# Performance work log

Hardware: AMD Instinct MI355X
Metric: run time of the kernel (lower is better)

Reference implementation:

```python
import math
import jax, jax.numpy as jnp
import numpy as np

N, E, D, B, S, H = 16384, 196608, 256, 256, 64, 8
DH = D // H
BN_INV = 1.0 / math.sqrt(1.0 + 1e-5)  # eval-mode BN: mean=0, var=1, eps=1e-5
LOG2 = math.log(2.0)


def _mlp(x, w1, b1, w2, b2):
    # Linear -> SiLU -> Linear
    return jax.nn.silu(x @ w1 + b1) @ w2 + b2


def _bn(x, g, b):
    # BatchNorm1d in eval mode with running_mean=0, running_var=1
    return x * (BN_INV * g) + b


def _graph_ln(x, g, b):
    # pyg LayerNorm(mode='graph') called with batch=None: normalize over all nodes+features
    mu = jnp.mean(x)
    xc = x - mu
    var = jnp.mean(xc * xc)
    return xc * jax.lax.rsqrt(var + 1e-5) * g + b


def _forward(x, edge_index, edge_attr,
             node_w1, node_b1, node_w2, node_b2,
             c_w1, c_b1, c_w2, c_b2,
             bn_e_g, bn_e_b, bn_h_g, bn_h_b,
             n1l_g, n1l_b, n1a_g, n1a_b, n2_g, n2_b,
             wq, bq, wk, bk, wv, bv, wo, bo,
             aff_w1, aff_b1, aff_w2, aff_b2,
             fn_g, fn_b, fc_w1, fc_b1, fc_w2, fc_b2):
    row, col = edge_index[0], edge_index[1]

    # ---- PotNetConvGate local branch ----
    # A, B, V, U MLPs (all take node features) computed with stacked weights [4,D,D]
    hid = jax.nn.silu(jnp.einsum('nd,kdf->knf', x, node_w1) + node_b1[:, None, :])
    node_out = jnp.einsum('knf,kfg->kng', hid, node_w2) + node_b2[:, None, :]
    h_A, h_B, h_V, h_U = node_out[0], node_out[1], node_out[2], node_out[3]
    e_C = _mlp(edge_attr, c_w1, c_b1, c_w2, c_b2)  # [E,D]

    score = jax.nn.relu(_bn(h_A[row] + h_B[col] + e_C, bn_e_g, bn_e_b))  # [E,D]
    e_new = edge_attr + score

    # pyg softmax over edges grouped by destination node (col), per channel
    m = jax.ops.segment_max(e_new, col, num_segments=N)        # [N,D]
    ex = jnp.exp(e_new - m[col])
    s = jax.ops.segment_sum(ex, col, num_segments=N)           # [N,D]
    gated = ex / (s[col] + 1e-16)

    msg = gated * (h_V[col] + e_new)
    aggr = jax.ops.segment_sum(msg, col, num_segments=N)       # [N,D]
    h_local = jax.nn.silu(x + _bn(h_U + aggr, bn_h_g, bn_h_b))
    # e_out = silu(e_new + edge_attr)  # edge output, not used downstream for node output
    h_local = _bn(h_local, n1l_g, n1l_b)  # norm1_local

    # ---- global Transformer branch (equal-size graphs -> dense reshape, full mask) ----
    hd = x.reshape(B, S, D)
    q = (hd @ wq + bq).reshape(B, S, H, DH).transpose(0, 2, 1, 3)
    k = (hd @ wk + bk).reshape(B, S, H, DH).transpose(0, 2, 1, 3)
    v = (hd @ wv + bv).reshape(B, S, H, DH).transpose(0, 2, 1, 3)
    att = jax.nn.softmax(jnp.einsum('bhqd,bhkd->bhqk', q, k) / math.sqrt(DH), axis=-1)
    o = jnp.einsum('bhqk,bhkd->bhqd', att, v).transpose(0, 2, 1, 3).reshape(B, S, D)
    h_attn = (o @ wo + bo).reshape(N, D)

    h_attn = _bn(h_attn + x, n1a_g, n1a_b)  # norm1_attn
    t = jax.nn.gelu(h_attn @ aff_w1 + aff_b1, approximate=False) @ aff_w2 + aff_b2
    h_attn = _graph_ln(t + x, fn_g, fn_b)   # feed_norm

    # ---- fuse branches (mean over stacked outputs) ----
    h_new = (h_local + h_attn) * 0.5

    # ---- _ff_block: fc = Linear -> ShiftedSoftplus -> Linear ----
    ssp = jax.nn.softplus(h_new @ fc_w1 + fc_b1) - LOG2
    out = ssp @ fc_w2 + fc_b2
    return _bn(out + h_new, n2_g, n2_b)  # norm2


def setup_inputs():
    key = jax.random.key(0)
    ks = iter(jax.random.split(key, 64))
    sc = 1.0 / math.sqrt(D)
    def w(shape):
        return jax.random.normal(next(ks), shape, jnp.float32) * sc
    z = lambda *s: jnp.zeros(s, jnp.float32)
    o = lambda *s: jnp.ones(s, jnp.float32)
    return {
        'x': jax.random.normal(next(ks), (N, D), jnp.float32),
        'edge_index': jax.random.randint(next(ks), (2, E), 0, N, jnp.int32),
        'edge_attr': jax.random.normal(next(ks), (E, D), jnp.float32),
        'node_w1': w((4, D, D)), 'node_b1': z(4, D),
        'node_w2': w((4, D, D)), 'node_b2': z(4, D),
        'c_w1': w((D, D)), 'c_b1': z(D), 'c_w2': w((D, D)), 'c_b2': z(D),
        'bn_e_g': o(D), 'bn_e_b': z(D), 'bn_h_g': o(D), 'bn_h_b': z(D),
        'n1l_g': o(D), 'n1l_b': z(D), 'n1a_g': o(D), 'n1a_b': z(D),
        'n2_g': o(D), 'n2_b': z(D),
        'wq': w((D, D)), 'bq': z(D), 'wk': w((D, D)), 'bk': z(D),
        'wv': w((D, D)), 'bv': z(D), 'wo': w((D, D)), 'bo': z(D),
        'aff_w1': w((D, 2 * D)), 'aff_b1': z(2 * D),
        'aff_w2': w((2 * D, D)), 'aff_b2': z(D),
        'fn_g': o(D), 'fn_b': z(D),
        'fc_w1': w((D, 2 * D)), 'fc_b1': z(2 * D),
        'fc_w2': w((2 * D, D)), 'fc_b2': z(D),
    }


def reference(x, edge_index, edge_attr,
              node_w1, node_b1, node_w2, node_b2,
              c_w1, c_b1, c_w2, c_b2,
              bn_e_g, bn_e_b, bn_h_g, bn_h_b,
              n1l_g, n1l_b, n1a_g, n1a_b, n2_g, n2_b,
              wq, bq, wk, bk, wv, bv, wo, bo,
              aff_w1, aff_b1, aff_w2, aff_b2,
              fn_g, fn_b, fc_w1, fc_b1, fc_w2, fc_b2):
    return _forward(x, edge_index, edge_attr,
                    node_w1, node_b1, node_w2, node_b2,
                    c_w1, c_b1, c_w2, c_b2,
                    bn_e_g, bn_e_b, bn_h_g, bn_h_b,
                    n1l_g, n1l_b, n1a_g, n1a_b, n2_g, n2_b,
                    wq, bq, wk, bk, wv, bv, wo, bo,
                    aff_w1, aff_b1, aff_w2, aff_b2,
                    fn_g, fn_b, fc_w1, fc_b1, fc_w2, fc_b2)
```

## Files before the change

### kernel.cpp

```cpp
#include <hip/hip_runtime.h>
#include <hip/hip_bf16.h>
#include <stdint.h>

#define NN 16384
#define NE 196608
#define DD 256
#define ND 4194304
#define BNINV 0.9999950000374997f
#define LOG2F_ 0.6931471805599453f

typedef __attribute__((ext_vector_type(8))) short short8v;
typedef __attribute__((ext_vector_type(4))) float float4v;

__device__ __forceinline__ float b2f(__hip_bfloat16 v) { return __bfloat162float(v); }
__device__ __forceinline__ __hip_bfloat16 f2b(float v) { return __float2bfloat16(v); }

__device__ __forceinline__ void gl_lds16(const __hip_bfloat16* g, __hip_bfloat16* l) {
  __builtin_amdgcn_global_load_lds((const __attribute__((address_space(1))) void*)g,
                                   (__attribute__((address_space(3))) void*)l, 16, 0, 0);
}

__device__ __forceinline__ float rdf(const void* p, size_t i, int fl) {
  return fl ? b2f(((const __hip_bfloat16*)p)[i]) : ((const float*)p)[i];
}

#define OFF_WT    0ul
#define OFF_PB    2883584ul
#define OFF_XB    2899968ul
#define OFF_HN    11288576ul
#define OFF_HL    44843008ul
#define OFF_EN    162283520ul
#define OFF_QKV   262946816ul
#define OFF_O     313278464ul
#define OFF_HATTN 321667072ul
#define OFF_HIDN  330055680ul
#define OFF_U     346832896ul
#define OFF_HNEW  363610112ul
#define OFF_HNEWB 380387328ul
#define OFF_TAIL  388775936ul

#define PB_NB1   0
#define PB_NB2   1024
#define PB_CB1   2048
#define PB_CB2   2304
#define PB_QKVB  2560
#define PB_BO    3328
#define PB_AB1   3584
#define PB_AB2   4096
#define PB_FB1   4352
#define PB_FB2   4864
#define PB_BNEG  5120
#define PB_BNEB  5376
#define PB_BNHG  5632
#define PB_BNHB  5888
#define PB_N1LG  6144
#define PB_N1LB  6400
#define PB_N1AG  6656
#define PB_N1AB  6912
#define PB_N2G   7168
#define PB_N2B   7424
#define PB_FNG   7680
#define PB_FNB   7936

__global__ void probe_kernel(const uint32_t* bneg_raw, int* flag) {
  if (threadIdx.x == 0 && blockIdx.x == 0)
    *flag = (bneg_raw[0] == 0x3F803F80u) ? 1 : 0;
}

struct PJobs {
  const void* src[24];
  int off[24];
  int len[24];
};

__global__ void canon_params(PJobs jb, __hip_bfloat16* PB, const int* flagp) {
  const int fl = *flagp;
  const int j = blockIdx.x;
  const void* src = jb.src[j];
  const int off = jb.off[j], len = jb.len[j];
  for (int i = threadIdx.x; i < len; i += 256) PB[off + i] = f2b(rdf(src, i, fl));
}

__global__ void canon_x(const void* x, __hip_bfloat16* XB, const int* flagp) {
  const int fl = *flagp;
  const size_t i = (size_t)blockIdx.x * 256 + threadIdx.x;
  XB[i] = f2b(rdf(x, i, fl));
}

struct TJobsF {
  const void* src[18];
  __hip_bfloat16* dst[18];
  int R[18];
  int C[18];
  int RB[18];
};

__global__ void transpose_rb(TJobsF jb, const int* flagp) {
  __shared__ __hip_bfloat16 tile[32][33];
  const int fl = *flagp;
  const int j = blockIdx.z;
  const int R = jb.R[j], C = jb.C[j], RB = jb.RB[j];
  const int c0 = blockIdx.x * 32, r0 = blockIdx.y * 32;
  if (c0 >= C || r0 >= R) return;
  const void* src = jb.src[j];
  __hip_bfloat16* dst = jb.dst[j];
  const int tx = threadIdx.x, ty = threadIdx.y;
#pragma unroll
  for (int i = 0; i < 4; ++i)
    tile[ty + i * 8][tx] = f2b(rdf(src, (size_t)(RB + r0 + ty + i * 8) * C + c0 + tx, fl));
  __syncthreads();
#pragma unroll
  for (int i = 0; i < 4; ++i)
    dst[(long)(c0 + ty + i * 8) * R + r0 + tx] = tile[tx][ty + i * 8];
}

__global__ void prep_kernel(int* counts, double* stats) {
  const int i = blockIdx.x * blockDim.x + threadIdx.x;
  if (i < NN) counts[i] = 0;
  if (i == 0) counts[NN] = 0;
  if (i < 2) stats[i] = 0.0;
}

template <int ACT, int RES, int BNM, int OUTBF, int DUALOUT>
__global__ __launch_bounds__(256) void gemm_bt(
    const void* __restrict__ Avp, const __hip_bfloat16* __restrict__ Wt,
    const __hip_bfloat16* __restrict__ bias, const void* __restrict__ Res,
    const __hip_bfloat16* __restrict__ bng, const __hip_bfloat16* __restrict__ bnb,
    void* __restrict__ Cout, const int* __restrict__ flagp,
    int M, int N, int K, long boff, long az, long wz, long bz, long cz) {
  __shared__ __align__(16) __hip_bfloat16 sA[128 * 32];
  __shared__ __align__(16) __hip_bfloat16 sB[128 * 32];
  const int fl = DUALOUT ? *flagp : 1;
  const int z = blockIdx.z;
  const long aoff = boff + (long)z * az;
  const __hip_bfloat16* Ab = (const __hip_bfloat16*)Avp + aoff;
  Wt += (long)z * wz;
  bias += (long)z * bz;
  const long coff = (long)z * cz;
  const int tid = threadIdx.x;
  const int lane = tid & 63;
  const int wid = tid >> 6;
  const int wm = wid >> 1, wn = wid & 1;
  const int l16 = lane & 15, lq = lane >> 4;
  const long am0 = (long)blockIdx.y * 128;
  const long bn0 = (long)blockIdx.x * 128;

  float4v acc[4][4] = {};

  const int nK = K >> 5;
  for (int kb = 0; kb < nK; ++kb) {
#pragma unroll
    for (int r = 0; r < 2; ++r) {
      const int c = tid + r * 256;
      gl_lds16(Ab + (am0 + (c >> 2)) * K + kb * 32 + (c & 3) * 8, sA + c * 8);
      gl_lds16(Wt + (bn0 + (c >> 2)) * K + kb * 32 + (c & 3) * 8, sB + c * 8);
    }
    __syncthreads();
    const short* pA = (const short*)sA;
    const short* pB = (const short*)sB;
    short8v af[4], bv_[4];
#pragma unroll
    for (int mi = 0; mi < 4; ++mi)
      af[mi] = *(const short8v*)(pA + (wm * 64 + mi * 16 + l16) * 32 + lq * 8);
#pragma unroll
    for (int ni = 0; ni < 4; ++ni)
      bv_[ni] = *(const short8v*)(pB + (wn * 64 + ni * 16 + l16) * 32 + lq * 8);
#pragma unroll
    for (int mi = 0; mi < 4; ++mi)
#pragma unroll
      for (int ni = 0; ni < 4; ++ni)
        acc[mi][ni] =
            __builtin_amdgcn_mfma_f32_16x16x32_bf16(af[mi], bv_[ni], acc[mi][ni], 0, 0, 0);
    __syncthreads();
  }

  const __hip_bfloat16* Rb = (const __hip_bfloat16*)Res;
  const float* Rf = (const float*)Res;
#pragma unroll
  for (int mi = 0; mi < 4; ++mi) {
#pragma unroll
    for (int ni = 0; ni < 4; ++ni) {
#pragma unroll
      for (int r = 0; r < 4; ++r) {
        const long row = am0 + wm * 64 + mi * 16 + lq * 4 + r;
        const long col = bn0 + wn * 64 + ni * 16 + l16;
        float v = acc[mi][ni][r] + b2f(bias[col]);
        if (ACT == 1) v = v / (1.f + __expf(-v));
        else if (ACT == 2) v = 0.5f * v * (1.f + erff(v * 0.7071067811865476f));
        else if (ACT == 3) v = (v > 15.f ? v : log1pf(__expf(v))) - LOG2F_;
        if (RES == 1) v += b2f(Rb[row * N + col]);
        else if (RES == 2) v += Rf[row * N + col];
        if (BNM) v = v * (BNINV * b2f(bng[col])) + b2f(bnb[col]);
        if (DUALOUT) {
          if (fl) ((__hip_bfloat16*)Cout)[coff + row * N + col] = f2b(v);
          else ((float*)Cout)[coff + row * N + col] = v;
        } else if (OUTBF) {
          ((__hip_bfloat16*)Cout)[coff + row * N + col] = f2b(v);
        } else {
          ((float*)Cout)[coff + row * N + col] = v;
        }
      }
    }
  }
}

template <int EPI, int ASRC>
__global__ __launch_bounds__(256) void mlp_fused(
    const void* __restrict__ Avp, const __hip_bfloat16* __restrict__ W1t,
    const __hip_bfloat16* __restrict__ b1, const __hip_bfloat16* __restrict__ W2t,
    const __hip_bfloat16* __restrict__ b2, __hip_bfloat16* __restrict__ Out,
    const int* __restrict__ ei, const void* __restrict__ eattr,
    const __hip_bfloat16* __restrict__ HA, __hip_bfloat16* __restrict__ EN,
    const __hip_bfloat16* __restrict__ PB, const int* __restrict__ perm,
    const int* __restrict__ flagp, long wz, long cz) {
  __shared__ __align__(16) __hip_bfloat16 sW[256 * 32];
  __shared__ __align__(16) __hip_bfloat16 sH[64 * 264];
  const int fl = (ASRC == 1) ? *flagp : 1;
  const int z = blockIdx.z;
  W1t += (long)z * wz;
  W2t += (long)z * wz;
  b1 += z * 256;
  b2 += z * 256;
  const int tid = threadIdx.x;
  const int lane = tid & 63;
  const int wn = tid >> 6;
  const int l16 = lane & 15, lq = lane >> 4;
  const long m0 = (long)blockIdx.y * 64;
  const __hip_bfloat16* Ab = (const __hip_bfloat16*)Avp;
  const float* Af = (const float*)Avp;

  float4v acc[4][4] = {};

  for (int kb = 0; kb < 8; ++kb) {
    if (ASRC == 1 && fl == 0) {
      const int arow = tid >> 2, ko = (tid & 3) * 8;
      const float* ap = Af + (m0 + arow) * 256 + kb * 32 + ko;
      const float4v f0 = *(const float4v*)ap;
      const float4v f1 = *(const float4v*)(ap + 4);
      short8v s;
#pragma unroll
      for (int i = 0; i < 4; ++i) {
        __hip_bfloat16 h0 = f2b(f0[i]), h1 = f2b(f1[i]);
        s[i] = *(short*)&h0;
        s[4 + i] = *(short*)&h1;
      }
      ((short8v*)sH)[tid] = s;
    } else {
      gl_lds16(Ab + (m0 + (tid >> 2)) * 256 + kb * 32 + (tid & 3) * 8, sH + tid * 8);
    }
#pragma unroll
    for (int r = 0; r < 4; ++r) {
      const int c2 = r * 256 + tid;
      gl_lds16(W1t + (c2 >> 2) * 256 + kb * 32 + (c2 & 3) * 8, sW + c2 * 8);
    }
    __syncthreads();
    short8v af[4], bf_[4];
#pragma unroll
    for (int mi = 0; mi < 4; ++mi)
      af[mi] = *(const short8v*)((const short*)sH + (mi * 16 + l16) * 32 + lq * 8);
#pragma unroll
    for (int ni = 0; ni < 4; ++ni)
      bf_[ni] = *(const short8v*)((const short*)sW + (wn * 64 + ni * 16 + l16) * 32 + lq * 8);
#pragma unroll
    for (int mi = 0; mi < 4; ++mi)
#pragma unroll
      for (int ni = 0; ni < 4; ++ni)
        acc[mi][ni] =
            __builtin_amdgcn_mfma_f32_16x16x32_bf16(af[mi], bf_[ni], acc[mi][ni], 0, 0, 0);
    __syncthreads();
  }

  {
    short* hp = (short*)sH;
#pragma unroll
    for (int mi = 0; mi < 4; ++mi)
#pragma unroll
      for (int ni = 0; ni < 4; ++ni)
#pragma unroll
        for (int r = 0; r < 4; ++r) {
          const int row = mi * 16 + lq * 4 + r;
          const int col = wn * 64 + ni * 16 + l16;
          float v = acc[mi][ni][r] + b2f(b1[col]);
          v = v / (1.f + __expf(-v));
          __hip_bfloat16 hb = f2b(v);
          hp[row * 264 + col] = *(short*)&hb;
          acc[mi][ni][r] = 0.f;
        }
  }
  __syncthreads();

  for (int kb = 0; kb < 8; ++kb) {
#pragma unroll
    for (int r = 0; r < 4; ++r) {
      const int c2 = r * 256 + tid;
      gl_lds16(W2t + (c2 >> 2) * 256 + kb * 32 + (c2 & 3) * 8, sW + c2 * 8);
    }
    __syncthreads();
    short8v af[4], bf_[4];
#pragma unroll
    for (int mi = 0; mi < 4; ++mi)
      af[mi] = *(const short8v*)((const short*)sH + (mi * 16 + l16) * 264 + kb * 32 + lq * 8);
#pragma unroll
    for (int ni = 0; ni < 4; ++ni)
      bf_[ni] = *(const short8v*)((const short*)sW + (wn * 64 + ni * 16 + l16) * 32 + lq * 8);
#pragma unroll
    for (int mi = 0; mi < 4; ++mi)
#pragma unroll
      for (int ni = 0; ni < 4; ++ni)
        acc[mi][ni] =
            __builtin_amdgcn_mfma_f32_16x16x32_bf16(af[mi], bf_[ni], acc[mi][ni], 0, 0, 0);
    __syncthreads();
  }

  if (EPI == 0) {
#pragma unroll
    for (int mi = 0; mi < 4; ++mi)
#pragma unroll
      for (int ni = 0; ni < 4; ++ni)
#pragma unroll
        for (int r = 0; r < 4; ++r) {
          const long row = m0 + mi * 16 + lq * 4 + r;
          const int col = wn * 64 + ni * 16 + l16;
          Out[(long)z * cz + row * 256 + col] = f2b(acc[mi][ni][r] + b2f(b2[col]));
        }
  } else {
    const __hip_bfloat16* HB = HA + (size_t)ND;
#pragma unroll
    for (int mi = 0; mi < 4; ++mi)
#pragma unroll
      for (int r = 0; r < 4; ++r) {
        const long ge = m0 + mi * 16 + lq * 4 + r;
        const int rr = ei[ge];
        const int cc = ei[NE + ge];
        const long pe = perm[ge];
#pragma unroll
        for (int ni = 0; ni < 4; ++ni) {
          const int col = wn * 64 + ni * 16 + l16;
          float v = acc[mi][ni][r] + b2f(b2[col]);
          v += b2f(HA[(size_t)rr * DD + col]) + b2f(HB[(size_t)cc * DD + col]);
          v = v * (BNINV * b2f(PB[PB_BNEG + col])) + b2f(PB[PB_BNEB + col]);
          v = fmaxf(v, 0.f);
          v += rdf(eattr, (size_t)ge * DD + col, fl);
          EN[(size_t)pe * DD + col] = f2b(v);
        }
      }
  }
}

__global__ void count_kernel(const int* __restrict__ ei, int* __restrict__ counts) {
  const int e = blockIdx.x * 256 + threadIdx.x;
  if (e < NE) atomicAdd(&counts[ei[NE + e]], 1);
}

__global__ __launch_bounds__(1024) void scan_kernel(int* __restrict__ counts,
                                                    int* __restrict__ cursor) {
  __shared__ int part[1024];
  const int t = threadIdx.x;
  const int base = t * 16;
  int ss = 0;
#pragma unroll
  for (int i = 0; i < 16; ++i) ss += counts[base + i];
  part[t] = ss;
  __syncthreads();
  for (int off = 1; off < 1024; off <<= 1) {
    int v = (t >= off) ? part[t - off] : 0;
    __syncthreads();
    part[t] += v;
    __syncthreads();
  }
  int run = part[t] - ss;
  for (int i = 0; i < 16; ++i) {
    const int cv = counts[base + i];
    counts[base + i] = run;
    cursor[base + i] = run;
    run += cv;
  }
  if (t == 1023) counts[NN] = run;
}

__global__ void scatter_kernel(const int* __restrict__ ei, int* __restrict__ cursor,
                               int* __restrict__ perm) {
  const int e = blockIdx.x * 256 + threadIdx.x;
  if (e < NE) {
    const int p = atomicAdd(&cursor[ei[NE + e]], 1);
    perm[e] = p;
  }
}

__global__ __launch_bounds__(256) void segment_kernel(
    const int* __restrict__ offs, const __hip_bfloat16* __restrict__ EN,
    const __hip_bfloat16* __restrict__ hV, const __hip_bfloat16* __restrict__ hU,
    const __hip_bfloat16* __restrict__ XB, const __hip_bfloat16* __restrict__ PB,
    float* __restrict__ hlocal) {
  const int n = blockIdx.x;
  const int d = threadIdx.x;
  const int beg = offs[n], end = offs[n + 1];
  float sa = 0.f, sb = 0.f;
  int p = beg;
  for (; p + 4 <= end; p += 4) {
    const float v0 = b2f(EN[(size_t)(p + 0) * DD + d]);
    const float v1 = b2f(EN[(size_t)(p + 1) * DD + d]);
    const float v2 = b2f(EN[(size_t)(p + 2) * DD + d]);
    const float v3 = b2f(EN[(size_t)(p + 3) * DD + d]);
    const float e0 = __expf(v0), e1 = __expf(v1), e2 = __expf(v2), e3 = __expf(v3);
    sa += (e0 + e1) + (e2 + e3);
    sb += (e0 * v0 + e1 * v1) + (e2 * v2 + e3 * v3);
  }
  for (; p < end; ++p) {
    const float v = b2f(EN[(size_t)p * DD + d]);
    const float e = __expf(v);
    sa += e;
    sb += e * v;
  }
  const float hv = b2f(hV[(size_t)n * DD + d]);
  const float ag = (hv * sa + sb) / (sa + 1e-16f);
  const float t1 =
      (b2f(hU[(size_t)n * DD + d]) + ag) * (BNINV * b2f(PB[PB_BNHG + d])) + b2f(PB[PB_BNHB + d]);
  float s1 = b2f(XB[(size_t)n * DD + d]) + t1;
  s1 = s1 / (1.f + __expf(-s1));
  s1 = s1 * (BNINV * b2f(PB[PB_N1LG + d])) + b2f(PB[PB_N1LB + d]);
  hlocal[(size_t)n * DD + d] = s1;
}

__global__ __launch_bounds__(256) void attn_kernel(const float* __restrict__ QKV,
                                                   __hip_bfloat16* __restrict__ O) {
  __shared__ float sq[64][33], sk[64][33], sv[64][33];
  __shared__ float sp[64][65];
  const int bh = blockIdx.x;
  const int b = bh >> 3, h = bh & 7;
  const int tid = threadIdx.x;
  const float* Q = QKV;
  const float* Kp = QKV + (size_t)ND;
  const float* Vp = QKV + 2 * (size_t)ND;
#pragma unroll
  for (int j = 0; j < 8; ++j) {
    const int idx = j * 256 + tid;
    const int s = idx >> 5, dh = idx & 31;
    const size_t ga = ((size_t)(b * 64 + s)) * DD + h * 32 + dh;
    sq[s][dh] = Q[ga];
    sk[s][dh] = Kp[ga];
    sv[s][dh] = Vp[ga];
  }
  __syncthreads();
  const int row = tid >> 2, l4 = tid & 3;
  float qr[32];
#pragma unroll
  for (int d = 0; d < 32; ++d) qr[d] = sq[row][d];
  float sc[16];
  float mx = -1e30f;
#pragma unroll
  for (int jj = 0; jj < 16; ++jj) {
    const int j = l4 * 16 + jj;
    float dot = 0.f;
#pragma unroll
    for (int d = 0; d < 32; ++d) dot += qr[d] * sk[j][d];
    dot *= 0.17677669529663687f;
    sc[jj] = dot;
    mx = fmaxf(mx, dot);
  }
  mx = fmaxf(mx, __shfl_xor(mx, 1));
  mx = fmaxf(mx, __shfl_xor(mx, 2));
  float se = 0.f;
#pragma unroll
  for (int jj = 0; jj < 16; ++jj) {
    sc[jj] = __expf(sc[jj] - mx);
    se += sc[jj];
  }
  se += __shfl_xor(se, 1);
  se += __shfl_xor(se, 2);
  const float inv = 1.f / se;
#pragma unroll
  for (int jj = 0; jj < 16; ++jj) sp[row][l4 * 16 + jj] = sc[jj] * inv;
  __syncthreads();
#pragma unroll
  for (int k8 = 0; k8 < 8; ++k8) {
    const int dh = l4 * 8 + k8;
    float acc = 0.f;
#pragma unroll
    for (int j = 0; j < 64; ++j) acc += sp[row][j] * sv[j][dh];
    O[((size_t)(b * 64 + row)) * DD + h * 32 + dh] = f2b(acc);
  }
}

__global__ __launch_bounds__(256) void stats_kernel(const float* __restrict__ U,
                                                    double* __restrict__ st) {
  double s = 0.0, s2 = 0.0;
  for (size_t i = (size_t)blockIdx.x * 256 + threadIdx.x; i < (size_t)ND;
       i += (size_t)gridDim.x * 256) {
    const double v = (double)U[i];
    s += v;
    s2 += v * v;
  }
  for (int o = 32; o > 0; o >>= 1) {
    s += __shfl_down(s, o);
    s2 += __shfl_down(s2, o);
  }
  __shared__ double wred[4][2];
  const int lane = threadIdx.x & 63, w = threadIdx.x >> 6;
  if (lane == 0) {
    wred[w][0] = s;
    wred[w][1] = s2;
  }
  __syncthreads();
  if (threadIdx.x == 0) {
    double a = 0, bb = 0;
    for (int i = 0; i < 4; ++i) {
      a += wred[i][0];
      bb += wred[i][1];
    }
    atomicAdd(&st[0], a);
    atomicAdd(&st[1], bb);
  }
}

__global__ void finalize_stats(double* st) {
  if (threadIdx.x == 0 && blockIdx.x == 0) {
    const double mu = st[0] / (double)ND;
    const double var = st[1] / (double)ND - mu * mu;
    float* f = (float*)(st + 2);
    f[0] = (float)mu;
    f[1] = (float)(1.0 / sqrt(var + 1e-5));
  }
}

__global__ void hnew_kernel(const float* __restrict__ U, const float* __restrict__ hlocal,
                            const double* __restrict__ st, const __hip_bfloat16* __restrict__ PB,
                            float* __restrict__ HNEW, __hip_bfloat16* __restrict__ HNEWB) {
  const size_t i = (size_t)blockIdx.x * 256 + threadIdx.x;
  const float* f = (const float*)(st + 2);
  const float mu = f[0], rs = f[1];
  const int d = (int)(i & 255);
  const float ha = (U[i] - mu) * rs * b2f(PB[PB_FNG + d]) + b2f(PB[PB_FNB + d]);
  const float hn = 0.5f * (hlocal[i] + ha);
  HNEW[i] = hn;
  HNEWB[i] = f2b(hn);
}

extern "C" void kernel_launch(void* const* d_in, const int* in_sizes, int n_in, void* d_out,
                              int out_size, void* d_ws, size_t ws_size, hipStream_t stream) {
  (void)in_sizes; (void)n_in; (void)out_size; (void)ws_size;
  const void* x = d_in[0];
  const int* ei = (const int*)d_in[1];
  const void* eattr = d_in[2];

  uint8_t* ws = (uint8_t*)d_ws;
  __hip_bfloat16* WT = (__hip_bfloat16*)(ws + OFF_WT);
  __hip_bfloat16* PB = (__hip_bfloat16*)(ws + OFF_PB);
  __hip_bfloat16* XB = (__hip_bfloat16*)(ws + OFF_XB);
  __hip_bfloat16* HN = (__hip_bfloat16*)(ws + OFF_HN);
  float* HL = (float*)(ws + OFF_HL);
  __hip_bfloat16* EN = (__hip_bfloat16*)(ws + OFF_EN);
  float* QKV = (float*)(ws + OFF_QKV);
  __hip_bfloat16* O = (__hip_bfloat16*)(ws + OFF_O);
  __hip_bfloat16* HATTN = (__hip_bfloat16*)(ws + OFF_HATTN);
  __hip_bfloat16* HIDN = (__hip_bfloat16*)(ws + OFF_HIDN);
  float* U = (float*)(ws + OFF_U);
  float* HNEW = (float*)(ws + OFF_HNEW);
  __hip_bfloat16* HNEWB = (__hip_bfloat16*)(ws + OFF_HNEWB);
  uint8_t* tail = ws + OFF_TAIL;
  int* counts = (int*)tail;
  int* cursor = (int*)(tail + 66048ul);
  int* perm = (int*)(tail + 132096ul);
  double* stats = (double*)(tail + 918528ul);
  int* flag = (int*)(tail + 918592ul);

  probe_kernel<<<1, 64, 0, stream>>>((const uint32_t*)d_in[11], flag);

  PJobs pj;
  {
    const int srcidx[24] = {4, 6, 8, 10, 22, 24, 26, 28, 30, 32, 36, 38,
                            11, 12, 13, 14, 15, 16, 17, 18, 19, 20, 33, 34};
    const int dstoff[24] = {PB_NB1, PB_NB2, PB_CB1, PB_CB2, PB_QKVB, PB_QKVB + 256,
                            PB_QKVB + 512, PB_BO, PB_AB1, PB_AB2, PB_FB1, PB_FB2,
                            PB_BNEG, PB_BNEB, PB_BNHG, PB_BNHB, PB_N1LG, PB_N1LB,
                            PB_N1AG, PB_N1AB, PB_N2G, PB_N2B, PB_FNG, PB_FNB};
    const int lens[24] = {1024, 1024, 256, 256, 256, 256, 256, 256, 512, 256, 512, 256,
                          256, 256, 256, 256, 256, 256, 256, 256, 256, 256, 256, 256};
    for (int i = 0; i < 24; ++i) {
      pj.src[i] = d_in[srcidx[i]];
      pj.off[i] = dstoff[i];
      pj.len[i] = lens[i];
    }
  }
  canon_params<<<24, 256, 0, stream>>>(pj, PB, flag);
  canon_x<<<NN, 256, 0, stream>>>(x, XB, flag);

  TJobsF jf;
  for (int j = 0; j < 4; ++j) {
    jf.src[j] = d_in[3]; jf.dst[j] = WT + j * 65536;
    jf.R[j] = 256; jf.C[j] = 256; jf.RB[j] = j * 256;
    jf.src[4 + j] = d_in[5]; jf.dst[4 + j] = WT + 262144 + j * 65536;
    jf.R[4 + j] = 256; jf.C[4 + j] = 256; jf.RB[4 + j] = j * 256;
  }
  {
    const int widx[10] = {7, 9, 21, 23, 25, 27, 29, 31, 35, 37};
    const long wdst[10] = {524288, 589824, 655360, 720896, 786432, 851968,
                           917504, 1048576, 1179648, 1310720};
    const int wR[10] = {256, 256, 256, 256, 256, 256, 256, 512, 256, 512};
    const int wC[10] = {256, 256, 256, 256, 256, 256, 512, 256, 512, 256};
    for (int j = 0; j < 10; ++j) {
      jf.src[8 + j] = d_in[widx[j]]; jf.dst[8 + j] = WT + wdst[j];
      jf.R[8 + j] = wR[j]; jf.C[8 + j] = wC[j]; jf.RB[8 + j] = 0;
    }
  }
  transpose_rb<<<dim3(16, 16, 18), dim3(32, 8), 0, stream>>>(jf, flag);

  prep_kernel<<<64, 256, 0, stream>>>(counts, stats);

  count_kernel<<<768, 256, 0, stream>>>(ei, counts);
  scan_kernel<<<1, 1024, 0, stream>>>(counts, cursor);
  scatter_kernel<<<768, 256, 0, stream>>>(ei, cursor, perm);

  mlp_fused<0, 0><<<dim3(1, 256, 4), 256, 0, stream>>>(
      XB, WT, PB + PB_NB1, WT + 262144, PB + PB_NB2, HN,
      nullptr, nullptr, nullptr, nullptr, nullptr, nullptr, flag, 65536, ND);

  mlp_fused<1, 1><<<dim3(1, 3072, 1), 256, 0, stream>>>(
      eattr, WT + 524288, PB + PB_CB1, WT + 589824, PB + PB_CB2, nullptr,
      ei, eattr, HN, EN, PB, perm, flag, 0, 0);

  segment_kernel<<<NN, 256, 0, stream>>>(counts, EN, HN + 2 * (size_t)ND,
                                         HN + 3 * (size_t)ND, XB, PB, HL);

  gemm_bt<0, 0, 0, 0, 0><<<dim3(2, 128, 3), 256, 0, stream>>>(
      XB, WT + 655360, PB + PB_QKVB, nullptr, nullptr, nullptr, QKV, flag,
      NN, DD, DD, 0, 0, 65536, 256, ND);
  attn_kernel<<<2048, 256, 0, stream>>>(QKV, O);
  gemm_bt<0, 1, 1, 1, 0><<<dim3(2, 128, 1), 256, 0, stream>>>(
      O, WT + 851968, PB + PB_BO, XB, PB + PB_N1AG, PB + PB_N1AB, HATTN, flag,
      NN, DD, DD, 0, 0, 0, 0, 0);

  gemm_bt<2, 0, 0, 1, 0><<<dim3(4, 128, 1), 256, 0, stream>>>(
      HATTN, WT + 917504, PB + PB_AB1, nullptr, nullptr, nullptr, HIDN, flag,
      NN, 512, DD, 0, 0, 0, 0, 0);
  gemm_bt<0, 1, 0, 0, 0><<<dim3(2, 128, 1), 256, 0, stream>>>(
      HIDN, WT + 1048576, PB + PB_AB2, XB, nullptr, nullptr, U, flag,
      NN, DD, 512, 0, 0, 0, 0, 0);

  stats_kernel<<<1024, 256, 0, stream>>>(U, stats);
  finalize_stats<<<1, 64, 0, stream>>>(stats);
  hnew_kernel<<<NN, 256, 0, stream>>>(U, HL, stats, PB, HNEW, HNEWB);

  gemm_bt<3, 0, 0, 1, 0><<<dim3(4, 128, 1), 256, 0, stream>>>(
      HNEWB, WT + 1179648, PB + PB_FB1, nullptr, nullptr, nullptr, HIDN, flag,
      NN, 512, DD, 0, 0, 0, 0, 0);
  gemm_bt<0, 2, 1, 1, 1><<<dim3(2, 128, 1), 256, 0, stream>>>(
      HIDN, WT + 1310720, PB + PB_FB2, HNEW, PB + PB_N2G, PB + PB_N2B, d_out, flag,
      NN, DD, 512, 0, 0, 0, 0, 0);
}
```

Baseline: 899.2 us.

## Load MFMA fragments directly from global memory instead of staging through LDS

Both the generic GEMM and the fused MLP kernel stop copying A and weight tiles into shared memory with global_load_lds. Each wave now reads its MFMA operand fragments straight from global memory into registers, which removes the per-K-step barriers and LDS traffic, and the loops are unrolled by two. In exchange, operand tiles shared across waves are fetched redundantly through the caches, and the strided 16-byte row reads may coalesce less well.

```diff
diff --git a/kernel.cpp b/kernel.cpp
--- a/kernel.cpp
+++ b/kernel.cpp
@@ -14,11 +14,6 @@
 
 __device__ __forceinline__ float b2f(__hip_bfloat16 v) { return __bfloat162float(v); }
 __device__ __forceinline__ __hip_bfloat16 f2b(float v) { return __float2bfloat16(v); }
-
-__device__ __forceinline__ void gl_lds16(const __hip_bfloat16* g, __hip_bfloat16* l) {
-  __builtin_amdgcn_global_load_lds((const __attribute__((address_space(1))) void*)g,
-                                   (__attribute__((address_space(3))) void*)l, 16, 0, 0);
-}
 
 __device__ __forceinline__ float rdf(const void* p, size_t i, int fl) {
   return fl ? b2f(((const __hip_bfloat16*)p)[i]) : ((const float*)p)[i];
@@ -128,8 +123,6 @@
     const __hip_bfloat16* __restrict__ bng, const __hip_bfloat16* __restrict__ bnb,
     void* __restrict__ Cout, const int* __restrict__ flagp,
     int M, int N, int K, long boff, long az, long wz, long bz, long cz) {
-  __shared__ __align__(16) __hip_bfloat16 sA[128 * 32];
-  __shared__ __align__(16) __hip_bfloat16 sB[128 * 32];
   const int fl = DUALOUT ? *flagp : 1;
   const int z = blockIdx.z;
   const long aoff = boff + (long)z * az;
@@ -148,30 +141,21 @@
   float4v acc[4][4] = {};
 
   const int nK = K >> 5;
+#pragma unroll 2
   for (int kb = 0; kb < nK; ++kb) {
-#pragma unroll
-    for (int r = 0; r < 2; ++r) {
-      const int c = tid + r * 256;
-      gl_lds16(Ab + (am0 + (c >> 2)) * K + kb * 32 + (c & 3) * 8, sA + c * 8);
-      gl_lds16(Wt + (bn0 + (c >> 2)) * K + kb * 32 + (c & 3) * 8, sB + c * 8);
-    }
-    __syncthreads();
-    const short* pA = (const short*)sA;
-    const short* pB = (const short*)sB;
     short8v af[4], bv_[4];
 #pragma unroll
     for (int mi = 0; mi < 4; ++mi)
-      af[mi] = *(const short8v*)(pA + (wm * 64 + mi * 16 + l16) * 32 + lq * 8);
+      af[mi] = *(const short8v*)(Ab + (am0 + wm * 64 + mi * 16 + l16) * K + kb * 32 + lq * 8);
 #pragma unroll
     for (int ni = 0; ni < 4; ++ni)
-      bv_[ni] = *(const short8v*)(pB + (wn * 64 + ni * 16 + l16) * 32 + lq * 8);
+      bv_[ni] = *(const short8v*)(Wt + (bn0 + wn * 64 + ni * 16 + l16) * K + kb * 32 + lq * 8);
 #pragma unroll
     for (int mi = 0; mi < 4; ++mi)
 #pragma unroll
       for (int ni = 0; ni < 4; ++ni)
         acc[mi][ni] =
             __builtin_amdgcn_mfma_f32_16x16x32_bf16(af[mi], bv_[ni], acc[mi][ni], 0, 0, 0);
-    __syncthreads();
   }
 
   const __hip_bfloat16* Rb = (const __hip_bfloat16*)Res;
@@ -213,7 +197,6 @@
     const __hip_bfloat16* __restrict__ HA, __hip_bfloat16* __restrict__ EN,
     const __hip_bfloat16* __restrict__ PB, const int* __restrict__ perm,
     const int* __restrict__ flagp, long wz, long cz) {
-  __shared__ __align__(16) __hip_bfloat16 sW[256 * 32];
   __shared__ __align__(16) __hip_bfloat16 sH[64 * 264];
   const int fl = (ASRC == 1) ? *flagp : 1;
   const int z = blockIdx.z;
@@ -231,43 +214,38 @@
 
   float4v acc[4][4] = {};
 
+#pragma unroll 2
   for (int kb = 0; kb < 8; ++kb) {
+    short8v af[4], bf_[4];
     if (ASRC == 1 && fl == 0) {
-      const int arow = tid >> 2, ko = (tid & 3) * 8;
-      const float* ap = Af + (m0 + arow) * 256 + kb * 32 + ko;
-      const float4v f0 = *(const float4v*)ap;
-      const float4v f1 = *(const float4v*)(ap + 4);
-      short8v s;
-#pragma unroll
-      for (int i = 0; i < 4; ++i) {
-        __hip_bfloat16 h0 = f2b(f0[i]), h1 = f2b(f1[i]);
-        s[i] = *(short*)&h0;
-        s[4 + i] = *(short*)&h1;
+#pragma unroll
+      for (int mi = 0; mi < 4; ++mi) {
+        const float* ap = Af + (m0 + mi * 16 + l16) * 256 + kb * 32 + lq * 8;
+        const float4v f0 = *(const float4v*)ap;
+        const float4v f1 = *(const float4v*)(ap + 4);
+        short8v s;
+#pragma unroll
+        for (int i = 0; i < 4; ++i) {
+          __hip_bfloat16 h0 = f2b(f0[i]), h1 = f2b(f1[i]);
+          s[i] = *(short*)&h0;
+          s[4 + i] = *(short*)&h1;
+        }
+        af[mi] = s;
       }
-      ((short8v*)sH)[tid] = s;
     } else {
-      gl_lds16(Ab + (m0 + (tid >> 2)) * 256 + kb * 32 + (tid & 3) * 8, sH + tid * 8);
+#pragma unroll
+      for (int mi = 0; mi < 4; ++mi)
+        af[mi] = *(const short8v*)(Ab + (m0 + mi * 16 + l16) * 256 + kb * 32 + lq * 8);
     }
 #pragma unroll
-    for (int r = 0; r < 4; ++r) {
-      const int c2 = r * 256 + tid;
-      gl_lds16(W1t + (c2 >> 2) * 256 + kb * 32 + (c2 & 3) * 8, sW + c2 * 8);
-    }
-    __syncthreads();
-    short8v af[4], bf_[4];
-#pragma unroll
-    for (int mi = 0; mi < 4; ++mi)
-      af[mi] = *(const short8v*)((const short*)sH + (mi * 16 + l16) * 32 + lq * 8);
-#pragma unroll
     for (int ni = 0; ni < 4; ++ni)
-      bf_[ni] = *(const short8v*)((const short*)sW + (wn * 64 + ni * 16 + l16) * 32 + lq * 8);
+      bf_[ni] = *(const short8v*)(W1t + (wn * 64 + ni * 16 + l16) * 256 + kb * 32 + lq * 8);
 #pragma unroll
     for (int mi = 0; mi < 4; ++mi)
 #pragma unroll
       for (int ni = 0; ni < 4; ++ni)
         acc[mi][ni] =
             __builtin_amdgcn_mfma_f32_16x16x32_bf16(af[mi], bf_[ni], acc[mi][ni], 0, 0, 0);
-    __syncthreads();
   }
 
   {
@@ -289,27 +267,21 @@
   }
   __syncthreads();
 
+#pragma unroll 2
   for (int kb = 0; kb < 8; ++kb) {
-#pragma unroll
-    for (int r = 0; r < 4; ++r) {
-      const int c2 = r * 256 + tid;
-      gl_lds16(W2t + (c2 >> 2) * 256 + kb * 32 + (c2 & 3) * 8, sW + c2 * 8);
-    }
-    __syncthreads();
     short8v af[4], bf_[4];
 #pragma unroll
     for (int mi = 0; mi < 4; ++mi)
       af[mi] = *(const short8v*)((const short*)sH + (mi * 16 + l16) * 264 + kb * 32 + lq * 8);
 #pragma unroll
     for (int ni = 0; ni < 4; ++ni)
-      bf_[ni] = *(const short8v*)((const short*)sW + (wn * 64 + ni * 16 + l16) * 32 + lq * 8);
+      bf_[ni] = *(const short8v*)(W2t + (wn * 64 + ni * 16 + l16) * 256 + kb * 32 + lq * 8);
 #pragma unroll
     for (int mi = 0; mi < 4; ++mi)
 #pragma unroll
       for (int ni = 0; ni < 4; ++ni)
         acc[mi][ni] =
             __builtin_amdgcn_mfma_f32_16x16x32_bf16(af[mi], bf_[ni], acc[mi][ni], 0, 0, 0);
-    __syncthreads();
   }
 
   if (EPI == 0) {
```

Result: slower. 1.322 ms (+47.1%).

## Double-buffer LDS tiles in gemm and fused MLP kernels to overlap loads

Applied to the files above, without the earlier changes.

Adds two-stage LDS buffering to the generic GEMM and the fused two-layer MLP kernel. The next K-slice of A and weights is issued into the alternate buffer before the MFMAs on the current slice, and one barrier per iteration replaces two. This is meant to hide global-to-LDS latency behind compute. The trade-off is doubled LDS use for the weight and tile buffers, which may lower occupancy. The fp32 input path is now prefetched into registers and converted after compute.

```diff
diff --git a/kernel.cpp b/kernel.cpp
--- a/kernel.cpp
+++ b/kernel.cpp
@@ -22,6 +22,26 @@
 
 __device__ __forceinline__ float rdf(const void* p, size_t i, int fl) {
   return fl ? b2f(((const __hip_bfloat16*)p)[i]) : ((const float*)p)[i];
+}
+
+__device__ __forceinline__ short8v cvt8(float4v f0, float4v f1) {
+  short8v s;
+#pragma unroll
+  for (int i = 0; i < 4; ++i) {
+    __hip_bfloat16 h0 = f2b(f0[i]), h1 = f2b(f1[i]);
+    s[i] = *(short*)&h0;
+    s[4 + i] = *(short*)&h1;
+  }
+  return s;
+}
+
+__device__ __forceinline__ void stage_w(const __hip_bfloat16* W, __hip_bfloat16* buf,
+                                        int kb, int tid) {
+#pragma unroll
+  for (int r = 0; r < 4; ++r) {
+    const int c2 = r * 256 + tid;
+    gl_lds16(W + (c2 >> 2) * 256 + kb * 32 + (c2 & 3) * 8, buf + c2 * 8);
+  }
 }
 
 #define OFF_WT    0ul
@@ -128,8 +148,8 @@
     const __hip_bfloat16* __restrict__ bng, const __hip_bfloat16* __restrict__ bnb,
     void* __restrict__ Cout, const int* __restrict__ flagp,
     int M, int N, int K, long boff, long az, long wz, long bz, long cz) {
-  __shared__ __align__(16) __hip_bfloat16 sA[128 * 32];
-  __shared__ __align__(16) __hip_bfloat16 sB[128 * 32];
+  __shared__ __align__(16) __hip_bfloat16 sA[2][128 * 32];
+  __shared__ __align__(16) __hip_bfloat16 sB[2][128 * 32];
   const int fl = DUALOUT ? *flagp : 1;
   const int z = blockIdx.z;
   const long aoff = boff + (long)z * az;
@@ -148,16 +168,27 @@
   float4v acc[4][4] = {};
 
   const int nK = K >> 5;
+#pragma unroll
+  for (int r = 0; r < 2; ++r) {
+    const int c = tid + r * 256;
+    gl_lds16(Ab + (am0 + (c >> 2)) * K + (c & 3) * 8, sA[0] + c * 8);
+    gl_lds16(Wt + (bn0 + (c >> 2)) * K + (c & 3) * 8, sB[0] + c * 8);
+  }
+  __syncthreads();
+
   for (int kb = 0; kb < nK; ++kb) {
-#pragma unroll
-    for (int r = 0; r < 2; ++r) {
-      const int c = tid + r * 256;
-      gl_lds16(Ab + (am0 + (c >> 2)) * K + kb * 32 + (c & 3) * 8, sA + c * 8);
-      gl_lds16(Wt + (bn0 + (c >> 2)) * K + kb * 32 + (c & 3) * 8, sB + c * 8);
+    const int cur = kb & 1;
+    if (kb + 1 < nK) {
+      const int nx = cur ^ 1;
+#pragma unroll
+      for (int r = 0; r < 2; ++r) {
+        const int c = tid + r * 256;
+        gl_lds16(Ab + (am0 + (c >> 2)) * K + (kb + 1) * 32 + (c & 3) * 8, sA[nx] + c * 8);
+        gl_lds16(Wt + (bn0 + (c >> 2)) * K + (kb + 1) * 32 + (c & 3) * 8, sB[nx] + c * 8);
+      }
     }
-    __syncthreads();
-    const short* pA = (const short*)sA;
-    const short* pB = (const short*)sB;
+    const short* pA = (const short*)sA[cur];
+    const short* pB = (const short*)sB[cur];
     short8v af[4], bv_[4];
 #pragma unroll
     for (int mi = 0; mi < 4; ++mi)
@@ -171,7 +202,7 @@
       for (int ni = 0; ni < 4; ++ni)
         acc[mi][ni] =
             __builtin_amdgcn_mfma_f32_16x16x32_bf16(af[mi], bv_[ni], acc[mi][ni], 0, 0, 0);
-    __syncthreads();
+    if (kb + 1 < nK) __syncthreads();
   }
 
   const __hip_bfloat16* Rb = (const __hip_bfloat16*)Res;
@@ -213,7 +244,7 @@
     const __hip_bfloat16* __restrict__ HA, __hip_bfloat16* __restrict__ EN,
     const __hip_bfloat16* __restrict__ PB, const int* __restrict__ perm,
     const int* __restrict__ flagp, long wz, long cz) {
-  __shared__ __align__(16) __hip_bfloat16 sW[256 * 32];
+  __shared__ __align__(16) __hip_bfloat16 sW[2][256 * 32];
   __shared__ __align__(16) __hip_bfloat16 sH[64 * 264];
   const int fl = (ASRC == 1) ? *flagp : 1;
   const int z = blockIdx.z;
@@ -228,45 +259,51 @@
   const long m0 = (long)blockIdx.y * 64;
   const __hip_bfloat16* Ab = (const __hip_bfloat16*)Avp;
   const float* Af = (const float*)Avp;
+  const int arow = tid >> 2, ako = (tid & 3) * 8;
 
   float4v acc[4][4] = {};
 
+  if (ASRC == 1 && fl == 0) {
+    const float* ap = Af + (m0 + arow) * 256 + ako;
+    ((short8v*)sH)[tid] = cvt8(*(const float4v*)ap, *(const float4v*)(ap + 4));
+  } else {
+    gl_lds16(Ab + (m0 + arow) * 256 + ako, sH + tid * 8);
+  }
+  stage_w(W1t, sW[0], 0, tid);
+  __syncthreads();
+
   for (int kb = 0; kb < 8; ++kb) {
-    if (ASRC == 1 && fl == 0) {
-      const int arow = tid >> 2, ko = (tid & 3) * 8;
-      const float* ap = Af + (m0 + arow) * 256 + kb * 32 + ko;
-      const float4v f0 = *(const float4v*)ap;
-      const float4v f1 = *(const float4v*)(ap + 4);
-      short8v s;
-#pragma unroll
-      for (int i = 0; i < 4; ++i) {
-        __hip_bfloat16 h0 = f2b(f0[i]), h1 = f2b(f1[i]);
-        s[i] = *(short*)&h0;
-        s[4 + i] = *(short*)&h1;
+    const int cur = kb & 1;
+    float4v pf0, pf1;
+    int pend = 0;
+    if (kb < 7) {
+      if (ASRC == 1 && fl == 0) {
+        const float* ap = Af + (m0 + arow) * 256 + (kb + 1) * 32 + ako;
+        pf0 = *(const float4v*)ap;
+        pf1 = *(const float4v*)(ap + 4);
+        pend = 1;
+      } else {
+        gl_lds16(Ab + (m0 + arow) * 256 + (kb + 1) * 32 + ako,
+                 sH + (cur ^ 1) * 2048 + tid * 8);
       }
-      ((short8v*)sH)[tid] = s;
-    } else {
-      gl_lds16(Ab + (m0 + (tid >> 2)) * 256 + kb * 32 + (tid & 3) * 8, sH + tid * 8);
+      stage_w(W1t, sW[cur ^ 1], kb + 1, tid);
     }
-#pragma unroll
-    for (int r = 0; r < 4; ++r) {
-      const int c2 = r * 256 + tid;
-      gl_lds16(W1t + (c2 >> 2) * 256 + kb * 32 + (c2 & 3) * 8, sW + c2 * 8);
-    }
-    __syncthreads();
+    const short* pA = (const short*)(sH + cur * 2048);
+    const short* pW = (const short*)sW[cur];
     short8v af[4], bf_[4];
 #pragma unroll
     for (int mi = 0; mi < 4; ++mi)
-      af[mi] = *(const short8v*)((const short*)sH + (mi * 16 + l16) * 32 + lq * 8);
+      af[mi] = *(const short8v*)(pA + (mi * 16 + l16) * 32 + lq * 8);
 #pragma unroll
     for (int ni = 0; ni < 4; ++ni)
-      bf_[ni] = *(const short8v*)((const short*)sW + (wn * 64 + ni * 16 + l16) * 32 + lq * 8);
+      bf_[ni] = *(const short8v*)(pW + (wn * 64 + ni * 16 + l16) * 32 + lq * 8);
 #pragma unroll
     for (int mi = 0; mi < 4; ++mi)
 #pragma unroll
       for (int ni = 0; ni < 4; ++ni)
         acc[mi][ni] =
             __builtin_amdgcn_mfma_f32_16x16x32_bf16(af[mi], bf_[ni], acc[mi][ni], 0, 0, 0);
+    if (pend) ((short8v*)(sH + (cur ^ 1) * 2048))[tid] = cvt8(pf0, pf1);
     __syncthreads();
   }
 
@@ -287,29 +324,27 @@
           acc[mi][ni][r] = 0.f;
         }
   }
+  stage_w(W2t, sW[0], 0, tid);
   __syncthreads();
 
   for (int kb = 0; kb < 8; ++kb) {
-#pragma unroll
-    for (int r = 0; r < 4; ++r) {
-      const int c2 = r * 256 + tid;
-      gl_lds16(W2t + (c2 >> 2) * 256 + kb * 32 + (c2 & 3) * 8, sW + c2 * 8);
-    }
-    __syncthreads();
+    const int cur = kb & 1;
+    if (kb < 7) stage_w(W2t, sW[cur ^ 1], kb + 1, tid);
+    const short* pW = (const short*)sW[cur];
     short8v af[4], bf_[4];
 #pragma unroll
     for (int mi = 0; mi < 4; ++mi)
       af[mi] = *(const short8v*)((const short*)sH + (mi * 16 + l16) * 264 + kb * 32 + lq * 8);
 #pragma unroll
     for (int ni = 0; ni < 4; ++ni)
-      bf_[ni] = *(const short8v*)((const short*)sW + (wn * 64 + ni * 16 + l16) * 32 + lq * 8);
+      bf_[ni] = *(const short8v*)(pW + (wn * 64 + ni * 16 + l16) * 32 + lq * 8);
 #pragma unroll
     for (int mi = 0; mi < 4; ++mi)
 #pragma unroll
       for (int ni = 0; ni < 4; ++ni)
         acc[mi][ni] =
             __builtin_amdgcn_mfma_f32_16x16x32_bf16(af[mi], bf_[ni], acc[mi][ni], 0, 0, 0);
-    __syncthreads();
+    if (kb < 7) __syncthreads();
   }
 
   if (EPI == 0) {
```

Result: slower. 938.4 us (+4.4%).
